# Kernel optimization log

Measured on AMD Instinct MI355X. Metric: run time of the kernel, lower is better.

The kernel has to match this reference:

```python
import jax, jax.numpy as jnp
import numpy as np

H = 32; L = 4; HEADS = 8; VC = 16; BIG = 1e9

def _unit(v):
    return v * jax.lax.rsqrt(jnp.sum(v * v, -1, keepdims=True) + 1e-8)

def _dihedrals(bb):
    n = bb.shape[0]
    X = bb[:, :3].reshape(n * 3, 3)
    U = _unit(X[1:] - X[:-1])
    u2, u1, u0 = U[:-2], U[1:-1], U[2:]
    n2 = _unit(jnp.cross(u2, u1)); n1 = _unit(jnp.cross(u1, u0))
    cosD = jnp.clip(jnp.sum(n2 * n1, -1), -1 + 1e-6, 1 - 1e-6)
    D = jnp.sign(jnp.sum(u2 * n1, -1)) * jnp.arccos(cosD)
    D = jnp.pad(D, (1, 2)).reshape(n, 3)
    return jnp.concatenate([jnp.cos(D), jnp.sin(D)], -1)

def _orientations(x):
    f = jnp.pad(_unit(x[1:] - x[:-1]), ((0, 1), (0, 0)))
    b = jnp.pad(_unit(x[:-1] - x[1:]), ((1, 0), (0, 0)))
    return jnp.stack([f, b], -2)

def _virtual_cb(bb):
    n_, ca, c = bb[:, 0], bb[:, 1], bb[:, 2]
    b = ca - n_; cc = c - ca; a = jnp.cross(b, cc)
    return -0.58273431 * a + 0.56802827 * b - 0.54067466 * cc + ca

def _rbf(d, nbin=16, dmax=20.0):
    mu = jnp.linspace(0.0, dmax, nbin); sig = dmax / nbin
    return jnp.exp(-(((d[..., None] - mu) / sig) ** 2))

def _pos_emb(didx, nemb=16):
    freq = jnp.exp(jnp.arange(0, nemb, 2, dtype=jnp.float32) * (-np.log(10000.0) / nemb))
    ang = didx[..., None].astype(jnp.float32) * freq
    return jnp.concatenate([jnp.cos(ang), jnp.sin(ang)], -1)

def _edge_rot(vec):
    # per-edge rotation aligning edge direction to e_y (equiformer-style)
    nrm = _unit(vec)
    helper = jnp.where(jnp.abs(nrm[..., 2:3]) > 0.99, jnp.array([1.0, 0.0, 0.0]), jnp.array([0.0, 0.0, 1.0]))
    z = _unit(jnp.cross(nrm, helper))
    x = jnp.cross(nrm, z)
    return jnp.stack([x, nrm, z], axis=-2)

def _rot(R, x):
    return jnp.concatenate([x[..., :1, :], jnp.einsum('...ij,...jc->...ic', R, x[..., 1:, :])], -2)

def _rot_inv(R, x):
    return jnp.concatenate([x[..., :1, :], jnp.einsum('...ji,...jc->...ic', R, x[..., 1:, :])], -2)

def _norm_so3(x, g0, b0, g1):
    x0 = x[..., 0, :]; x1 = x[..., 1:, :]
    mu = jnp.mean(x0, -1, keepdims=True)
    var = jnp.var(x0, -1, keepdims=True)
    y0 = (x0 - mu) * jax.lax.rsqrt(var + 1e-6) * g0 + b0
    y1 = x1 * jax.lax.rsqrt(jnp.mean(x1 * x1, (-2, -1), keepdims=True) + 1e-6) * g1
    return jnp.concatenate([y0[..., None, :], y1], -2)

def _project(xin, nbr, R, ef, rw1, rw2, ow):
    src = _rot(R, xin[nbr])                         # [N,k,4,Cin] gather + rotate into edge frame
    rad = jax.nn.silu(ef @ rw1) @ rw2               # [N,k,Cin] radial weights
    msg = _rot_inv(R, src * rad[..., None, :])      # rotate back to global frame
    return jnp.mean(msg, axis=1) @ ow               # [N,4,Cout]

def _forward(bb, latent, ln_g0, ln_b0, ln_g1, bb_rad_w1, bb_rad_w2, bb_out_w,
             lat_rad_w1, lat_rad_w2, lat_out_w, tln_g0, tln_b0, tln_g1,
             attn_w1, attn_w2, v_w, o_w, ffn_w1, ffn_w2, ffn_wg, ffn_v1,
             eu_w1, eu_w2, out_rad_w1, out_rad_w2, out_w,
             seq_w1, seq_b1, seq_w2, seq_b2, seq_w3, seq_b3, x_mask, n_per, k):
    N = bb.shape[0]
    Xca = bb[:, 1]
    # backbone SO3 features [N,4,7]: l=0 dihedrals (padded to 7), l=1 seven vectors
    dih = jnp.pad(_dihedrals(bb), ((0, 0), (0, 1)))
    vecs = jnp.concatenate([bb - Xca[:, None], _orientations(Xca),
                            (_virtual_cb(bb) - Xca)[:, None]], -2)
    bb_feat = jnp.concatenate([dih[:, None, :], jnp.nan_to_num(jnp.swapaxes(vecs, -1, -2))], 1)
    # kNN graph within each chain; masked residues pushed far away
    batch = jnp.arange(N) // n_per
    mx = jnp.where(x_mask[:, None], BIG, Xca)
    sq = jnp.sum(mx * mx, -1)
    d2 = sq[:, None] + sq[None, :] - 2.0 * (mx @ mx.T)
    bad = (batch[:, None] != batch[None, :]) | jnp.eye(N, dtype=bool)
    d2 = jnp.where(bad, BIG, d2)
    _, nbr = jax.lax.top_k(-d2, k)                  # [N,k] source indices per target
    edge_vec = Xca[:, None] - Xca[nbr]
    R = _edge_rot(edge_vec)                         # [N,k,3,3]
    dist = jnp.sqrt(jnp.sum(edge_vec * edge_vec, -1) + 1e-12)
    ef = jnp.concatenate([_rbf(dist), _pos_emb(nbr - jnp.arange(N)[:, None])], -1)  # [N,k,32]
    lat = _norm_so3(latent, ln_g0, ln_b0, ln_g1)
    x = jnp.concatenate([_project(bb_feat, nbr, R, ef, bb_rad_w1, bb_rad_w2, bb_out_w),
                         _project(lat, nbr, R, ef, lat_rad_w1, lat_rad_w2, lat_out_w)], -1)  # [N,4,H]
    for l in range(L):
        xl = _norm_so3(x, tln_g0[l], tln_b0[l], tln_g1[l])
        src = xl[nbr]                               # [N,k,4,H]
        feat = jnp.concatenate([src[..., 0, :],
                                jnp.broadcast_to(xl[:, None, 0, :], src[..., 0, :].shape),
                                ef], -1)            # [N,k,3H]
        alpha = jax.nn.softmax(jax.nn.silu(feat @ attn_w1[l]) @ attn_w2[l], axis=1)  # [N,k,heads]
        v = _rot_inv(R, _rot(R, src) @ v_w[l])      # [N,k,4,heads*vc]
        v = v.reshape(N, k, 4, HEADS, VC)
        agg = jnp.einsum('nkh,nkchv->nchv', alpha, v).reshape(N, 4, HEADS * VC)
        x = x + agg @ o_w[l]
        h = jax.nn.silu(x[:, 0, :] @ ffn_w1[l])
        gate = jax.nn.sigmoid(h @ ffn_wg[l])
        x = x + jnp.concatenate([(h @ ffn_w2[l])[:, None, :],
                                 (x[:, 1:, :] @ ffn_v1[l]) * gate[:, None, :]], 1)
        e_in = jnp.concatenate([ef, x[nbr][..., 0, :],
                                jnp.broadcast_to(x[:, None, 0, :], (N, k, H))], -1)
        ef = ef + jax.nn.silu(e_in @ eu_w1[l]) @ eu_w2[l]
    atoms = _project(x, nbr, R, ef, out_rad_w1, out_rad_w2, out_w)  # [N,4,91]
    decoded_latent = jnp.swapaxes(atoms[:, 1:4, :], -1, -2)         # [N,91,3]
    hh = jax.nn.relu(x[:, 0, :] @ seq_w1 + seq_b1)
    hh = jax.nn.relu(hh @ seq_w2 + seq_b2)
    seq_logits = jax.nn.log_softmax(hh @ seq_w3 + seq_b3, -1)
    return decoded_latent, seq_logits

def setup_inputs() -> dict:
    key = jax.random.key(0)
    N = 8192; n_per = 2048; k = 30
    keys = iter(jax.random.split(key, 64))
    def W(shape):
        fan = shape[-2] if len(shape) > 1 else shape[-1]
        return (jax.random.normal(next(keys), shape) / np.sqrt(fan)).astype(jnp.float32)
    inp = {
        'bb': (jax.random.normal(next(keys), (N, 4, 3)) * 3.0).astype(jnp.float32),
        'latent': jax.random.normal(next(keys), (N, 4, H), dtype=jnp.float32),
        'ln_g0': jnp.ones((H,), jnp.float32), 'ln_b0': jnp.zeros((H,), jnp.float32), 'ln_g1': jnp.ones((H,), jnp.float32),
        'bb_rad_w1': W((H, 64)), 'bb_rad_w2': W((64, 7)), 'bb_out_w': W((7, 16)),
        'lat_rad_w1': W((H, 64)), 'lat_rad_w2': W((64, H)), 'lat_out_w': W((H, 16)),
        'tln_g0': jnp.ones((L, H), jnp.float32), 'tln_b0': jnp.zeros((L, H), jnp.float32), 'tln_g1': jnp.ones((L, H), jnp.float32),
        'attn_w1': W((L, 3 * H, H)), 'attn_w2': W((L, H, HEADS)),
        'v_w': W((L, H, HEADS * VC)), 'o_w': W((L, HEADS * VC, H)),
        'ffn_w1': W((L, H, 2 * H)), 'ffn_w2': W((L, 2 * H, H)), 'ffn_wg': W((L, 2 * H, H)), 'ffn_v1': W((L, H, H)),
        'eu_w1': W((L, 3 * H, 2 * H)), 'eu_w2': W((L, 2 * H, H)),
        'out_rad_w1': W((H, 64)), 'out_rad_w2': W((64, H)), 'out_w': W((H, 91)),
        'seq_w1': W((H, 64)), 'seq_b1': jnp.zeros((64,), jnp.float32),
        'seq_w2': W((64, H)), 'seq_b2': jnp.zeros((H,), jnp.float32),
        'seq_w3': W((H, 20)), 'seq_b3': jnp.zeros((20,), jnp.float32),
        'x_mask': jnp.zeros((N,), bool), 'n_per': n_per, 'k': k,
    }
    return inp

def reference(bb, latent, ln_g0, ln_b0, ln_g1, bb_rad_w1, bb_rad_w2, bb_out_w,
              lat_rad_w1, lat_rad_w2, lat_out_w, tln_g0, tln_b0, tln_g1,
              attn_w1, attn_w2, v_w, o_w, ffn_w1, ffn_w2, ffn_wg, ffn_v1,
              eu_w1, eu_w2, out_rad_w1, out_rad_w2, out_w,
              seq_w1, seq_b1, seq_w2, seq_b2, seq_w3, seq_b3, x_mask, n_per, k):
    return _forward(bb, latent, ln_g0, ln_b0, ln_g1, bb_rad_w1, bb_rad_w2, bb_out_w,
                    lat_rad_w1, lat_rad_w2, lat_out_w, tln_g0, tln_b0, tln_g1,
                    attn_w1, attn_w2, v_w, o_w, ffn_w1, ffn_w2, ffn_wg, ffn_v1,
                    eu_w1, eu_w2, out_rad_w1, out_rad_w2, out_w,
                    seq_w1, seq_b1, seq_w2, seq_b2, seq_w3, seq_b3, x_mask, n_per, k)
```

## Files before the change

kernel.cpp:

```cpp
#include <hip/hip_runtime.h>
#include <math.h>

#define NRES 8192
#define NPER 2048
#define KNB  30
#define NEDGE (NRES*KNB)

__device__ __forceinline__ float siluf(float x){ return x / (1.0f + __expf(-x)); }

__global__ void k_pack(const float* __restrict__ bb, float4* __restrict__ ca){
  int n = blockIdx.x*256 + threadIdx.x;
  if(n >= NRES) return;
  float x=bb[n*12+3], y=bb[n*12+4], z=bb[n*12+5];
  ca[n] = make_float4(x,y,z, x*x+y*y+z*z);
}

__global__ void k_bbfeat(const float* __restrict__ bb, float* __restrict__ bbf){
  int n = blockIdx.x*256 + threadIdx.x;
  if(n >= NRES) return;
  const float* r = bb + n*12;
  float cax=r[3], cay=r[4], caz=r[5];
  float vx[7],vy[7],vz[7];
  for(int a=0;a<4;a++){ vx[a]=r[a*3]-cax; vy[a]=r[a*3+1]-cay; vz[a]=r[a*3+2]-caz; }
  if(n<NRES-1){
    float dx=bb[(n+1)*12+3]-cax, dy=bb[(n+1)*12+4]-cay, dz=bb[(n+1)*12+5]-caz;
    float s=rsqrtf(dx*dx+dy*dy+dz*dz+1e-8f);
    vx[4]=dx*s; vy[4]=dy*s; vz[4]=dz*s;
  } else { vx[4]=0.f; vy[4]=0.f; vz[4]=0.f; }
  if(n>0){
    float dx=bb[(n-1)*12+3]-cax, dy=bb[(n-1)*12+4]-cay, dz=bb[(n-1)*12+5]-caz;
    float s=rsqrtf(dx*dx+dy*dy+dz*dz+1e-8f);
    vx[5]=dx*s; vy[5]=dy*s; vz[5]=dz*s;
  } else { vx[5]=0.f; vy[5]=0.f; vz[5]=0.f; }
  {
    float bx=cax-r[0], by=cay-r[1], bz=caz-r[2];
    float cx=r[6]-cax, cy=r[7]-cay, cz=r[8]-caz;
    float axx=by*cz-bz*cy, ayy=bz*cx-bx*cz, azz=bx*cy-by*cx;
    vx[6]=-0.58273431f*axx+0.56802827f*bx-0.54067466f*cx;
    vy[6]=-0.58273431f*ayy+0.56802827f*by-0.54067466f*cy;
    vz[6]=-0.58273431f*azz+0.56802827f*bz-0.54067466f*cz;
  }
  float cD[3], sD[3];
  for(int t=0;t<3;t++){
    cD[t]=1.0f; sD[t]=0.0f;
    int f=3*n+t-1;
    if(f>=0 && f<3*NRES-3){
      float X[4][3];
      for(int q=0;q<4;q++){
        int m=f+q, rr=m/3, aa=m-rr*3;
        X[q][0]=bb[rr*12+aa*3]; X[q][1]=bb[rr*12+aa*3+1]; X[q][2]=bb[rr*12+aa*3+2];
      }
      float u2x=X[1][0]-X[0][0], u2y=X[1][1]-X[0][1], u2z=X[1][2]-X[0][2];
      float u1x=X[2][0]-X[1][0], u1y=X[2][1]-X[1][1], u1z=X[2][2]-X[1][2];
      float u0x=X[3][0]-X[2][0], u0y=X[3][1]-X[2][1], u0z=X[3][2]-X[2][2];
      float s2=rsqrtf(u2x*u2x+u2y*u2y+u2z*u2z+1e-8f); u2x*=s2; u2y*=s2; u2z*=s2;
      float s1=rsqrtf(u1x*u1x+u1y*u1y+u1z*u1z+1e-8f); u1x*=s1; u1y*=s1; u1z*=s1;
      float s0=rsqrtf(u0x*u0x+u0y*u0y+u0z*u0z+1e-8f); u0x*=s0; u0y*=s0; u0z*=s0;
      float n2x=u2y*u1z-u2z*u1y, n2y=u2z*u1x-u2x*u1z, n2z=u2x*u1y-u2y*u1x;
      float nn2=rsqrtf(n2x*n2x+n2y*n2y+n2z*n2z+1e-8f); n2x*=nn2; n2y*=nn2; n2z*=nn2;
      float n1x=u1y*u0z-u1z*u0y, n1y=u1z*u0x-u1x*u0z, n1z=u1x*u0y-u1y*u0x;
      float nn1=rsqrtf(n1x*n1x+n1y*n1y+n1z*n1z+1e-8f); n1x*=nn1; n1y*=nn1; n1z*=nn1;
      float dotn = n2x*n1x+n2y*n1y+n2z*n1z;
      float cosD = fminf(fmaxf(dotn, -1.0f+1e-6f), 1.0f-1e-6f);
      float sg = u2x*n1x+u2y*n1y+u2z*n1z;
      if(sg==0.0f){ cD[t]=1.0f; sD[t]=0.0f; }
      else {
        float sgn = (sg>0.0f)?1.0f:-1.0f;
        cD[t]=cosD;
        sD[t]=sgn*sqrtf(fmaxf(1.0f-cosD*cosD,0.0f));
      }
    }
  }
  float* o = bbf + n*28;
  o[0]=cD[0]; o[1]=cD[1]; o[2]=cD[2]; o[3]=sD[0]; o[4]=sD[1]; o[5]=sD[2]; o[6]=0.f;
  for(int c=0;c<7;c++){ o[7+c]=vx[c]; o[14+c]=vy[c]; o[21+c]=vz[c]; }
}

__global__ __launch_bounds__(256) void k_knn(const float4* __restrict__ ca, int* __restrict__ nbr){
  __shared__ float sx[NPER], sy[NPER], sz[NPER], sq[NPER];
  int wave = threadIdx.x>>6;
  int lane = threadIdx.x&63;
  int i = blockIdx.x*4 + wave;
  int batch = i / NPER;
  int base = batch*NPER;
  for(int t=threadIdx.x; t<NPER; t+=256){
    float4 c = ca[base+t];
    sx[t]=c.x; sy[t]=c.y; sz[t]=c.z; sq[t]=c.w;
  }
  __syncthreads();
  int il = i - base;
  float xi=sx[il], yi=sy[il], zi=sz[il], si=sq[il];
  float vals[32];
  float lmin = 1e30f; int larg = 0;
  #pragma unroll
  for(int t=0;t<32;t++){
    int j = t*64 + lane;
    float d2 = si + sq[j] - 2.0f*(xi*sx[j]+yi*sy[j]+zi*sz[j]);
    if(j==il) d2 = 1e30f;
    vals[t]=d2;
    if(d2 < lmin){ lmin=d2; larg=t; }
  }
  for(int it=0; it<KNB; it++){
    float v = lmin; int jg = larg*64 + lane;
    #pragma unroll
    for(int off=32; off>0; off>>=1){
      float vo = __shfl_xor(v, off, 64);
      int   jo = __shfl_xor(jg, off, 64);
      if(vo < v || (vo==v && jo<jg)){ v=vo; jg=jo; }
    }
    if(lane==0) nbr[i*KNB+it] = base + jg;
    if((jg&63)==lane){
      int targ = jg>>6;
      lmin = 1e30f; larg = 0;
      #pragma unroll
      for(int t=0;t<32;t++){
        if(t==targ) vals[t]=1e30f;
        if(vals[t]<lmin){ lmin=vals[t]; larg=t; }
      }
    }
  }
}

__global__ void k_edgefeat(const float4* __restrict__ ca, const int* __restrict__ nbr,
                           float* __restrict__ ef){
  int e = blockIdx.x*256 + threadIdx.x;
  if(e >= NEDGE) return;
  int n = e/KNB;
  int j = nbr[e];
  float4 cn = ca[n], cj = ca[j];
  float dx=cn.x-cj.x, dy=cn.y-cj.y, dz=cn.z-cj.z;
  float dist = sqrtf(dx*dx+dy*dy+dz*dz + 1e-12f);
  float* o = ef + (size_t)e*32;
  for(int m=0;m<16;m++){
    float mu = (20.0f/15.0f)*(float)m;
    float t = (dist-mu)*(1.0f/1.25f);
    o[m] = __expf(-t*t);
  }
  float didx = (float)(j - n);
  for(int m=0;m<8;m++){
    float freq = __expf(-1.1512925465f*(float)m);
    float ang = didx*freq;
    o[16+m]=cosf(ang); o[24+m]=sinf(ang);
  }
}

__global__ void k_norm(const float* __restrict__ in, float* __restrict__ out,
                       const float* __restrict__ g0, const float* __restrict__ b0,
                       const float* __restrict__ g1){
  int tid = blockIdx.x*256 + threadIdx.x;
  int n = tid >> 5, lane = tid & 31;
  if(n >= NRES) return;
  const float* xn = in + n*128;
  float x0 = xn[lane];
  float s = x0, s2 = x0*x0;
  for(int off=16; off>0; off>>=1){ s += __shfl_xor(s, off, 32); s2 += __shfl_xor(s2, off, 32); }
  float mu = s*(1.0f/32.0f);
  float var = s2*(1.0f/32.0f) - mu*mu;
  float y0 = (x0-mu)*rsqrtf(var+1e-6f)*g0[lane] + b0[lane];
  float v1 = xn[32+lane], v2 = xn[64+lane], v3 = xn[96+lane];
  float ss = v1*v1+v2*v2+v3*v3;
  for(int off=16; off>0; off>>=1){ ss += __shfl_xor(ss, off, 32); }
  float sc = rsqrtf(ss*(1.0f/96.0f) + 1e-6f);
  float g = g1[lane];
  out[n*128+lane]     = y0;
  out[n*128+32+lane]  = v1*sc*g;
  out[n*128+64+lane]  = v2*sc*g;
  out[n*128+96+lane]  = v3*sc*g;
}

__device__ __forceinline__ void load32(float* __restrict__ f, const float* __restrict__ src){
  const float4* s4 = (const float4*)src;
  #pragma unroll
  for(int q=0;q<8;q++){
    float4 v = s4[q];
    f[q*4+0]=v.x; f[q*4+1]=v.y; f[q*4+2]=v.z; f[q*4+3]=v.w;
  }
}

__global__ __launch_bounds__(256,4) void k_rad(const float* __restrict__ ef,
                     const float* __restrict__ bbw1, const float* __restrict__ bbw2,
                     const float* __restrict__ latw1, const float* __restrict__ latw2,
                     float* __restrict__ radbb, float* __restrict__ radlat){
  int e = blockIdx.x*256 + threadIdx.x;
  float f[32];
  load32(f, ef + (size_t)e*32);
  float h[64];
  #pragma unroll
  for(int o=0;o<64;o++) h[o]=0.f;
  #pragma unroll
  for(int c=0;c<32;c++){
    const float* w = bbw1 + c*64;
    #pragma unroll
    for(int o=0;o<64;o++) h[o] += f[c]*w[o];
  }
  float ab[7];
  #pragma unroll
  for(int t=0;t<7;t++) ab[t]=0.f;
  #pragma unroll
  for(int o=0;o<64;o++){
    float v = siluf(h[o]);
    const float* w2 = bbw2 + o*7;
    #pragma unroll
    for(int t=0;t<7;t++) ab[t] += v*w2[t];
  }
  {
    float4* rb4 = (float4*)(radbb + (size_t)e*8);
    rb4[0] = make_float4(ab[0],ab[1],ab[2],ab[3]);
    rb4[1] = make_float4(ab[4],ab[5],ab[6],0.f);
  }
  #pragma unroll
  for(int o=0;o<64;o++) h[o]=0.f;
  #pragma unroll
  for(int c=0;c<32;c++){
    const float* w = latw1 + c*64;
    #pragma unroll
    for(int o=0;o<64;o++) h[o] += f[c]*w[o];
  }
  float al[32];
  #pragma unroll
  for(int t=0;t<32;t++) al[t]=0.f;
  #pragma unroll
  for(int o=0;o<64;o++){
    float v = siluf(h[o]);
    const float* w2 = latw2 + o*32;
    #pragma unroll
    for(int t=0;t<32;t++) al[t] += v*w2[t];
  }
  float4* rl4 = (float4*)(radlat + (size_t)e*32);
  #pragma unroll
  for(int q=0;q<8;q++) rl4[q] = make_float4(al[q*4],al[q*4+1],al[q*4+2],al[q*4+3]);
}

__global__ __launch_bounds__(256) void k_init(const int* __restrict__ nbr,
                       const float* __restrict__ radbb, const float* __restrict__ radlat,
                       const float* __restrict__ bbf, const float* __restrict__ latn,
                       const float* __restrict__ bboutw, const float* __restrict__ latoutw,
                       const float* __restrict__ g0, const float* __restrict__ b0,
                       const float* __restrict__ g1,
                       float* __restrict__ x, float* __restrict__ xl){
  __shared__ float msgbb[4][32], msglat[4][128], xout[4][128];
  int g = threadIdx.x>>6, t = threadIdx.x&63;
  int n = blockIdx.x*4 + g;
  int t31 = t&31, t7 = t%7;
  float accL0=0.f, accL1=0.f, accB=0.f;
  for(int kk=0; kk<KNB; kk++){
    int e = n*KNB+kk;
    int j = nbr[e];
    float rl = radlat[(size_t)e*32 + t31];
    accL0 += latn[j*128+t]    * rl;
    accL1 += latn[j*128+64+t] * rl;
    if(t<28) accB += bbf[j*28+t]*radbb[(size_t)e*8 + t7];
  }
  msglat[g][t]=accL0*(1.0f/KNB); msglat[g][64+t]=accL1*(1.0f/KNB);
  if(t<28) msgbb[g][t]=accB*(1.0f/KNB);
  for(int half=0; half<2; half++){
    int e = half*64+t;
    int rrow = e>>5, c = e&31;
    float v=0.f;
    if(c<16){ for(int q=0;q<7;q++)  v += msgbb[g][rrow*7+q]*bboutw[q*16+c]; }
    else    { for(int q=0;q<32;q++) v += msglat[g][rrow*32+q]*latoutw[q*16+(c-16)]; }
    xout[g][e]=v;
    x[n*128+e]=v;
  }
  if(t<32){
    float x0=xout[g][t];
    float s=x0, s2=x0*x0;
    for(int off=16; off>0; off>>=1){ s+=__shfl_xor(s,off,32); s2+=__shfl_xor(s2,off,32); }
    float mu=s*(1.0f/32.0f), var=s2*(1.0f/32.0f)-mu*mu;
    float y0=(x0-mu)*rsqrtf(var+1e-6f)*g0[t]+b0[t];
    float v1=xout[g][32+t], v2=xout[g][64+t], v3=xout[g][96+t];
    float ss=v1*v1+v2*v2+v3*v3;
    for(int off=16; off>0; off>>=1) ss+=__shfl_xor(ss,off,32);
    float sc=rsqrtf(ss*(1.0f/96.0f)+1e-6f);
    float gg=g1[t];
    xl[n*128+t]=y0; xl[n*128+32+t]=v1*sc*gg; xl[n*128+64+t]=v2*sc*gg; xl[n*128+96+t]=v3*sc*gg;
  }
}

__global__ __launch_bounds__(256,4) void k_logits(const int* __restrict__ nbr, const float* __restrict__ xl,
                         const float* __restrict__ ef, const float* __restrict__ w1,
                         const float* __restrict__ w2, float* __restrict__ logits){
  int e = blockIdx.x*256 + threadIdx.x;
  int n = e/KNB;
  int j = nbr[e];
  float h[32];
  #pragma unroll
  for(int o=0;o<32;o++) h[o]=0.f;
  float f[32];
  load32(f, xl + (size_t)j*128);
  #pragma unroll
  for(int c=0;c<32;c++){
    const float* w = w1 + c*32;
    #pragma unroll
    for(int o=0;o<32;o++) h[o] += f[c]*w[o];
  }
  load32(f, xl + (size_t)n*128);
  #pragma unroll
  for(int c=0;c<32;c++){
    const float* w = w1 + (32+c)*32;
    #pragma unroll
    for(int o=0;o<32;o++) h[o] += f[c]*w[o];
  }
  load32(f, ef + (size_t)e*32);
  #pragma unroll
  for(int c=0;c<32;c++){
    const float* w = w1 + (64+c)*32;
    #pragma unroll
    for(int o=0;o<32;o++) h[o] += f[c]*w[o];
  }
  float acc[8];
  #pragma unroll
  for(int t=0;t<8;t++) acc[t]=0.f;
  #pragma unroll
  for(int o=0;o<32;o++){
    float v = siluf(h[o]);
    const float* w = w2 + o*8;
    #pragma unroll
    for(int t=0;t<8;t++) acc[t] += v*w[t];
  }
  float4* lg4 = (float4*)(logits + (size_t)e*8);
  lg4[0] = make_float4(acc[0],acc[1],acc[2],acc[3]);
  lg4[1] = make_float4(acc[4],acc[5],acc[6],acc[7]);
}

__global__ __launch_bounds__(256) void k_update(const int* __restrict__ nbr, const float* __restrict__ xl,
                         const float* __restrict__ logits, float* __restrict__ x,
                         float* __restrict__ xlout,
                         const float* __restrict__ vw, const float* __restrict__ ow,
                         const float* __restrict__ fw1, const float* __restrict__ fw2,
                         const float* __restrict__ fwg, const float* __restrict__ fv1,
                         const float* __restrict__ g0, const float* __restrict__ b0,
                         const float* __restrict__ g1){
  __shared__ float S_lg[4][240], S_m[4][8], S_inv[4][8];
  __shared__ float S_S[4][1024], S_agg[4][512], S_x[4][128];
  __shared__ float S_h[4][64], S_g[4][32], S_d0[4][32];
  int g = threadIdx.x>>6, t = threadIdx.x&63;
  int n = blockIdx.x*4 + g;
  for(int r=t; r<240; r+=64) S_lg[g][r] = logits[(size_t)n*240+r];
  if(t<8){
    float m=-1e30f;
    for(int kk=0;kk<KNB;kk++) m=fmaxf(m, S_lg[g][kk*8+t]);
    float s=0.f;
    for(int kk=0;kk<KNB;kk++) s += __expf(S_lg[g][kk*8+t]-m);
    S_m[g][t]=m; S_inv[g][t]=1.0f/s;
  }
  for(int r=t; r<240; r+=64){ int h=r&7; S_lg[g][r]=__expf(S_lg[g][r]-S_m[g][h])*S_inv[g][h]; }
  int hd = t>>3, i8 = t&7;
  const float4* xl4 = (const float4*)xl;
  float acc[16];
  for(int m=0;m<16;m++) acc[m]=0.f;
  for(int kk=0;kk<KNB;kk++){
    int j=nbr[n*KNB+kk];
    float a = S_lg[g][kk*8+hd];
    float4 b0v = xl4[j*32 + i8*4 + 0];
    float4 b1v = xl4[j*32 + i8*4 + 1];
    float4 b2v = xl4[j*32 + i8*4 + 2];
    float4 b3v = xl4[j*32 + i8*4 + 3];
    acc[0]+=a*b0v.x; acc[1]+=a*b0v.y; acc[2]+=a*b0v.z; acc[3]+=a*b0v.w;
    acc[4]+=a*b1v.x; acc[5]+=a*b1v.y; acc[6]+=a*b1v.z; acc[7]+=a*b1v.w;
    acc[8]+=a*b2v.x; acc[9]+=a*b2v.y; acc[10]+=a*b2v.z; acc[11]+=a*b2v.w;
    acc[12]+=a*b3v.x; acc[13]+=a*b3v.y; acc[14]+=a*b3v.z; acc[15]+=a*b3v.w;
  }
  for(int m=0;m<16;m++) S_S[g][hd*128 + i8*16 + m] = acc[m];
  for(int half=0; half<2; half++){
    int hv = half*64+t;
    int hh = hv>>4;
    float a0=0.f,a1=0.f,a2=0.f,a3=0.f;
    for(int c=0;c<32;c++){
      float w = vw[c*128+hv];
      a0 += S_S[g][hh*128 + c]*w;
      a1 += S_S[g][hh*128 + 32+c]*w;
      a2 += S_S[g][hh*128 + 64+c]*w;
      a3 += S_S[g][hh*128 + 96+c]*w;
    }
    S_agg[g][hv]=a0; S_agg[g][128+hv]=a1; S_agg[g][256+hv]=a2; S_agg[g][384+hv]=a3;
  }
  for(int half=0; half<2; half++){
    int e = half*64+t;
    int rrow = e>>5, c = e&31;
    float v = x[n*128+e];
    for(int hv=0;hv<128;hv++) v += S_agg[g][rrow*128+hv]*ow[hv*32+c];
    S_x[g][e]=v;
  }
  {
    float hs=0.f;
    for(int c=0;c<32;c++) hs += S_x[g][c]*fw1[c*64+t];
    S_h[g][t]=siluf(hs);
  }
  if(t<32){
    float gs=0.f, d0=0.f;
    for(int c=0;c<64;c++){ float hv=S_h[g][c]; gs += hv*fwg[c*32+t]; d0 += hv*fw2[c*32+t]; }
    S_g[g][t]=1.0f/(1.0f+__expf(-gs));
    S_d0[g][t]=d0;
  }
  for(int half=0; half<2; half++){
    int e = half*64+t;
    int rrow = e>>5, c = e&31;
    float xv = S_x[g][e], outv;
    if(rrow==0){ outv = xv + S_d0[g][c]; }
    else {
      float dv=0.f;
      for(int cc=0;cc<32;cc++) dv += S_x[g][rrow*32+cc]*fv1[cc*32+c];
      outv = xv + dv*S_g[g][c];
    }
    S_x[g][e]=outv;
    x[n*128+e]=outv;
  }
  if(t<32){
    float x0=S_x[g][t];
    float s=x0, s2=x0*x0;
    for(int off=16; off>0; off>>=1){ s+=__shfl_xor(s,off,32); s2+=__shfl_xor(s2,off,32); }
    float mu=s*(1.0f/32.0f), var=s2*(1.0f/32.0f)-mu*mu;
    float y0=(x0-mu)*rsqrtf(var+1e-6f)*g0[t]+b0[t];
    float v1=S_x[g][32+t], v2=S_x[g][64+t], v3=S_x[g][96+t];
    float ss=v1*v1+v2*v2+v3*v3;
    for(int off=16; off>0; off>>=1) ss+=__shfl_xor(ss,off,32);
    float sc=rsqrtf(ss*(1.0f/96.0f)+1e-6f);
    float gg=g1[t];
    xlout[n*128+t]=y0; xlout[n*128+32+t]=v1*sc*gg;
    xlout[n*128+64+t]=v2*sc*gg; xlout[n*128+96+t]=v3*sc*gg;
  }
}

__global__ __launch_bounds__(256,4) void k_efup(const int* __restrict__ nbr, const float* __restrict__ x,
                       const float* __restrict__ ew1, const float* __restrict__ ew2,
                       float* __restrict__ ef){
  int e = blockIdx.x*256 + threadIdx.x;
  int n = e/KNB;
  int j = nbr[e];
  float h[64];
  #pragma unroll
  for(int o=0;o<64;o++) h[o]=0.f;
  float f[32];
  load32(f, ef + (size_t)e*32);
  #pragma unroll
  for(int c=0;c<32;c++){
    const float* w = ew1 + c*64;
    #pragma unroll
    for(int o=0;o<64;o++) h[o] += f[c]*w[o];
  }
  load32(f, x + (size_t)j*128);
  #pragma unroll
  for(int c=0;c<32;c++){
    const float* w = ew1 + (32+c)*64;
    #pragma unroll
    for(int o=0;o<64;o++) h[o] += f[c]*w[o];
  }
  load32(f, x + (size_t)n*128);
  #pragma unroll
  for(int c=0;c<32;c++){
    const float* w = ew1 + (64+c)*64;
    #pragma unroll
    for(int o=0;o<64;o++) h[o] += f[c]*w[o];
  }
  float acc[32];
  #pragma unroll
  for(int t=0;t<32;t++) acc[t]=0.f;
  #pragma unroll
  for(int o=0;o<64;o++){
    float v = siluf(h[o]);
    const float* w = ew2 + o*32;
    #pragma unroll
    for(int t=0;t<32;t++) acc[t] += v*w[t];
  }
  load32(f, ef + (size_t)e*32);
  float4* e4 = (float4*)(ef + (size_t)e*32);
  #pragma unroll
  for(int q=0;q<8;q++){
    e4[q] = make_float4(f[q*4+0]+acc[q*4+0], f[q*4+1]+acc[q*4+1],
                        f[q*4+2]+acc[q*4+2], f[q*4+3]+acc[q*4+3]);
  }
}

__global__ __launch_bounds__(256,4) void k_orad(const float* __restrict__ ef,
                      const float* __restrict__ orw1, const float* __restrict__ orw2,
                      float* __restrict__ orad){
  int e = blockIdx.x*256 + threadIdx.x;
  float f[32];
  load32(f, ef + (size_t)e*32);
  float h[64];
  #pragma unroll
  for(int o=0;o<64;o++) h[o]=0.f;
  #pragma unroll
  for(int c=0;c<32;c++){
    const float* w = orw1 + c*64;
    #pragma unroll
    for(int o=0;o<64;o++) h[o] += f[c]*w[o];
  }
  float acc[32];
  #pragma unroll
  for(int t=0;t<32;t++) acc[t]=0.f;
  #pragma unroll
  for(int o=0;o<64;o++){
    float v = siluf(h[o]);
    const float* w = orw2 + o*32;
    #pragma unroll
    for(int t=0;t<32;t++) acc[t] += v*w[t];
  }
  float4* r4 = (float4*)(orad + (size_t)e*32);
  #pragma unroll
  for(int q=0;q<8;q++) r4[q] = make_float4(acc[q*4],acc[q*4+1],acc[q*4+2],acc[q*4+3]);
}

__global__ __launch_bounds__(256) void k_out(const int* __restrict__ nbr, const float* __restrict__ orad,
                      const float* __restrict__ x,
                      const float* __restrict__ outw,
                      const float* __restrict__ sw1, const float* __restrict__ sb1,
                      const float* __restrict__ sw2, const float* __restrict__ sb2,
                      const float* __restrict__ sw3, const float* __restrict__ sb3,
                      float* __restrict__ out, float* __restrict__ outseq){
  __shared__ float msg[4][128];
  __shared__ float h1[4][64], h2[4][32], lgs[4][20];
  int g = threadIdx.x>>6, t = threadIdx.x&63;
  int n = blockIdx.x*4 + g;
  int t31 = t&31;
  float acc0=0.f, acc1=0.f;
  for(int kk=0;kk<KNB;kk++){
    int e=n*KNB+kk;
    int j=nbr[e];
    float rl = orad[(size_t)e*32 + t31];
    acc0 += x[j*128+t]*rl;
    acc1 += x[j*128+64+t]*rl;
  }
  msg[g][t]=acc0*(1.0f/KNB); msg[g][64+t]=acc1*(1.0f/KNB);
  for(int o=t;o<91;o+=64){
    for(int rrow=1;rrow<4;rrow++){
      float s=0.f;
      for(int c=0;c<32;c++) s += msg[g][rrow*32+c]*outw[c*91+o];
      out[(size_t)n*273 + o*3 + (rrow-1)] = s;
    }
  }
  {
    float s=0.f;
    for(int c=0;c<32;c++) s += x[n*128+c]*sw1[c*64+t];
    h1[g][t]=fmaxf(s+sb1[t],0.f);
  }
  if(t<32){
    float s=0.f;
    for(int c=0;c<64;c++) s += h1[g][c]*sw2[c*32+t];
    h2[g][t]=fmaxf(s+sb2[t],0.f);
  }
  if(t<20){
    float s=0.f;
    for(int c=0;c<32;c++) s += h2[g][c]*sw3[c*20+t];
    lgs[g][t]=s+sb3[t];
  }
  if(t<20){
    float m=-1e30f;
    for(int c=0;c<20;c++) m=fmaxf(m,lgs[g][c]);
    float se=0.f;
    for(int c=0;c<20;c++) se += __expf(lgs[g][c]-m);
    outseq[(size_t)n*20+t]=lgs[g][t]-m-logf(se);
  }
}

extern "C" void kernel_launch(void* const* d_in, const int* in_sizes, int n_in,
                              void* d_out, int out_size, void* d_ws, size_t ws_size,
                              hipStream_t stream) {
  const float* bb      = (const float*)d_in[0];
  const float* latent  = (const float*)d_in[1];
  const float* ln_g0   = (const float*)d_in[2];
  const float* ln_b0   = (const float*)d_in[3];
  const float* ln_g1   = (const float*)d_in[4];
  const float* bbw1    = (const float*)d_in[5];
  const float* bbw2    = (const float*)d_in[6];
  const float* bboutw  = (const float*)d_in[7];
  const float* latw1   = (const float*)d_in[8];
  const float* latw2   = (const float*)d_in[9];
  const float* latoutw = (const float*)d_in[10];
  const float* tg0     = (const float*)d_in[11];
  const float* tb0     = (const float*)d_in[12];
  const float* tg1     = (const float*)d_in[13];
  const float* aw1     = (const float*)d_in[14];
  const float* aw2     = (const float*)d_in[15];
  const float* vw      = (const float*)d_in[16];
  const float* ow      = (const float*)d_in[17];
  const float* fw1     = (const float*)d_in[18];
  const float* fw2     = (const float*)d_in[19];
  const float* fwg     = (const float*)d_in[20];
  const float* fv1     = (const float*)d_in[21];
  const float* ew1     = (const float*)d_in[22];
  const float* ew2     = (const float*)d_in[23];
  const float* orw1    = (const float*)d_in[24];
  const float* orw2    = (const float*)d_in[25];
  const float* outw    = (const float*)d_in[26];
  const float* sw1     = (const float*)d_in[27];
  const float* sb1     = (const float*)d_in[28];
  const float* sw2     = (const float*)d_in[29];
  const float* sb2     = (const float*)d_in[30];
  const float* sw3     = (const float*)d_in[31];
  const float* sb3     = (const float*)d_in[32];
  float* outp = (float*)d_out;

  int*    nbr    = (int*)d_ws;
  float*  ef     = (float*)((char*)d_ws + 1024*1024);
  float*  xbuf   = ef   + (size_t)NEDGE*32;
  float*  xlA    = xbuf + (size_t)NRES*128;
  float*  xlB    = xlA  + (size_t)NRES*128;
  float*  bbf    = xlB  + (size_t)NRES*128;
  float*  logits = bbf  + (size_t)NRES*28;
  float4* ca     = (float4*)(logits + (size_t)NEDGE*8);
  float*  edgescratch = (float*)(ca + NRES);
  float*  radbb  = logits;
  float*  radlat = edgescratch;
  float*  orad   = edgescratch;

  k_pack    <<<NRES/256, 256, 0, stream>>>(bb, ca);
  k_bbfeat  <<<NRES/256, 256, 0, stream>>>(bb, bbf);
  k_knn     <<<NRES/4,   256, 0, stream>>>(ca, nbr);
  k_edgefeat<<<NEDGE/256, 256, 0, stream>>>(ca, nbr, ef);
  k_norm    <<<NRES*32/256, 256, 0, stream>>>(latent, xlA, ln_g0, ln_b0, ln_g1);
  k_rad     <<<NEDGE/256, 256, 0, stream>>>(ef, bbw1, bbw2, latw1, latw2, radbb, radlat);
  k_init    <<<NRES/4, 256, 0, stream>>>(nbr, radbb, radlat, bbf, xlA,
                                         bboutw, latoutw,
                                         tg0, tb0, tg1,
                                         xbuf, xlB);
  for(int l=0;l<4;l++){
    const float* xl_in  = (l&1) ? xlA : xlB;
    float*       xl_out = (l&1) ? xlB : xlA;
    int ln = (l+1<4) ? (l+1) : 3;
    k_logits <<<NEDGE/256, 256, 0, stream>>>(nbr, xl_in, ef, aw1+l*96*32, aw2+l*32*8, logits);
    k_update <<<NRES/4, 256, 0, stream>>>(nbr, xl_in, logits, xbuf, xl_out,
                                          vw+l*32*128, ow+l*128*32,
                                          fw1+l*32*64, fw2+l*64*32,
                                          fwg+l*64*32, fv1+l*32*32,
                                          tg0+ln*32, tb0+ln*32, tg1+ln*32);
    k_efup   <<<NEDGE/256, 256, 0, stream>>>(nbr, xbuf, ew1+l*96*64, ew2+l*64*32, ef);
  }
  k_orad<<<NEDGE/256, 256, 0, stream>>>(ef, orw1, orw2, orad);
  k_out <<<NRES/4, 256, 0, stream>>>(nbr, orad, xbuf, outw,
                                     sw1, sb1, sw2, sb2, sw3, sb3,
                                     outp, outp + (size_t)NRES*273);
}
```

Baseline: 1.329 ms.

## Fuse edge feature computation into radial MLP and speed up kNN selection

Removes the separate edge-feature kernel: k_rad now computes the RBF and positional features itself, uses them directly, and writes them to ef for later layers. This saves one launch and a read of ef. The kNN kernel now uses 512-thread blocks that share the staged coordinates across 8 queries. It also keeps per-group minima over four groups of 8 candidates, so each extraction rescans only one group instead of all 32 values. The costs are extra register pressure in k_rad and more branching in the kNN inner loop.

```diff
diff --git a/kernel.cpp b/kernel.cpp
--- a/kernel.cpp
+++ b/kernel.cpp
@@ -76,14 +76,14 @@
   for(int c=0;c<7;c++){ o[7+c]=vx[c]; o[14+c]=vy[c]; o[21+c]=vz[c]; }
 }
 
-__global__ __launch_bounds__(256) void k_knn(const float4* __restrict__ ca, int* __restrict__ nbr){
+__global__ __launch_bounds__(512) void k_knn(const float4* __restrict__ ca, int* __restrict__ nbr){
   __shared__ float sx[NPER], sy[NPER], sz[NPER], sq[NPER];
   int wave = threadIdx.x>>6;
   int lane = threadIdx.x&63;
-  int i = blockIdx.x*4 + wave;
+  int i = blockIdx.x*8 + wave;
   int batch = i / NPER;
   int base = batch*NPER;
-  for(int t=threadIdx.x; t<NPER; t+=256){
+  for(int t=threadIdx.x; t<NPER; t+=512){
     float4 c = ca[base+t];
     sx[t]=c.x; sy[t]=c.y; sz[t]=c.z; sq[t]=c.w;
   }
@@ -91,15 +91,22 @@
   int il = i - base;
   float xi=sx[il], yi=sy[il], zi=sz[il], si=sq[il];
   float vals[32];
-  float lmin = 1e30f; int larg = 0;
+  float gm[4]; int ga[4];
+  #pragma unroll
+  for(int grp=0;grp<4;grp++){ gm[grp]=1e30f; ga[grp]=grp*8; }
   #pragma unroll
   for(int t=0;t<32;t++){
     int j = t*64 + lane;
     float d2 = si + sq[j] - 2.0f*(xi*sx[j]+yi*sy[j]+zi*sz[j]);
     if(j==il) d2 = 1e30f;
     vals[t]=d2;
-    if(d2 < lmin){ lmin=d2; larg=t; }
-  }
+    int grp = t>>3;
+    if(d2 < gm[grp]){ gm[grp]=d2; ga[grp]=t; }
+  }
+  float lmin = gm[0]; int larg = ga[0];
+  if(gm[1]<lmin){ lmin=gm[1]; larg=ga[1]; }
+  if(gm[2]<lmin){ lmin=gm[2]; larg=ga[2]; }
+  if(gm[3]<lmin){ lmin=gm[3]; larg=ga[3]; }
   for(int it=0; it<KNB; it++){
     float v = lmin; int jg = larg*64 + lane;
     #pragma unroll
@@ -110,37 +117,24 @@
     }
     if(lane==0) nbr[i*KNB+it] = base + jg;
     if((jg&63)==lane){
-      int targ = jg>>6;
-      lmin = 1e30f; larg = 0;
+      int wt = jg>>6;
+      int grp = wt>>3;
       #pragma unroll
-      for(int t=0;t<32;t++){
-        if(t==targ) vals[t]=1e30f;
-        if(vals[t]<lmin){ lmin=vals[t]; larg=t; }
+      for(int g2=0; g2<4; g2++){
+        if(grp==g2){
+          #pragma unroll
+          for(int q=0;q<8;q++) if(g2*8+q==wt) vals[g2*8+q]=1e30f;
+          float m=1e30f; int a=g2*8;
+          #pragma unroll
+          for(int q=0;q<8;q++){ if(vals[g2*8+q]<m){ m=vals[g2*8+q]; a=g2*8+q; } }
+          gm[g2]=m; ga[g2]=a;
+        }
       }
+      lmin=gm[0]; larg=ga[0];
+      if(gm[1]<lmin){ lmin=gm[1]; larg=ga[1]; }
+      if(gm[2]<lmin){ lmin=gm[2]; larg=ga[2]; }
+      if(gm[3]<lmin){ lmin=gm[3]; larg=ga[3]; }
     }
-  }
-}
-
-__global__ void k_edgefeat(const float4* __restrict__ ca, const int* __restrict__ nbr,
-                           float* __restrict__ ef){
-  int e = blockIdx.x*256 + threadIdx.x;
-  if(e >= NEDGE) return;
-  int n = e/KNB;
-  int j = nbr[e];
-  float4 cn = ca[n], cj = ca[j];
-  float dx=cn.x-cj.x, dy=cn.y-cj.y, dz=cn.z-cj.z;
-  float dist = sqrtf(dx*dx+dy*dy+dz*dz + 1e-12f);
-  float* o = ef + (size_t)e*32;
-  for(int m=0;m<16;m++){
-    float mu = (20.0f/15.0f)*(float)m;
-    float t = (dist-mu)*(1.0f/1.25f);
-    o[m] = __expf(-t*t);
-  }
-  float didx = (float)(j - n);
-  for(int m=0;m<8;m++){
-    float freq = __expf(-1.1512925465f*(float)m);
-    float ang = didx*freq;
-    o[16+m]=cosf(ang); o[24+m]=sinf(ang);
   }
 }
 
@@ -177,13 +171,36 @@
   }
 }
 
-__global__ __launch_bounds__(256,4) void k_rad(const float* __restrict__ ef,
+__global__ __launch_bounds__(256,4) void k_rad(const float4* __restrict__ ca, const int* __restrict__ nbr,
                      const float* __restrict__ bbw1, const float* __restrict__ bbw2,
                      const float* __restrict__ latw1, const float* __restrict__ latw2,
+                     float* __restrict__ ef,
                      float* __restrict__ radbb, float* __restrict__ radlat){
   int e = blockIdx.x*256 + threadIdx.x;
+  int n = e/KNB;
+  int j = nbr[e];
+  float4 cn = ca[n], cj = ca[j];
+  float dx=cn.x-cj.x, dy=cn.y-cj.y, dz=cn.z-cj.z;
+  float dist = sqrtf(dx*dx+dy*dy+dz*dz + 1e-12f);
   float f[32];
-  load32(f, ef + (size_t)e*32);
+  #pragma unroll
+  for(int m=0;m<16;m++){
+    float mu = (20.0f/15.0f)*(float)m;
+    float t = (dist-mu)*(1.0f/1.25f);
+    f[m] = __expf(-t*t);
+  }
+  float didx = (float)(j - n);
+  #pragma unroll
+  for(int m=0;m<8;m++){
+    float freq = __expf(-1.1512925465f*(float)m);
+    float ang = didx*freq;
+    f[16+m]=cosf(ang); f[24+m]=sinf(ang);
+  }
+  {
+    float4* o4 = (float4*)(ef + (size_t)e*32);
+    #pragma unroll
+    for(int q=0;q<8;q++) o4[q] = make_float4(f[q*4],f[q*4+1],f[q*4+2],f[q*4+3]);
+  }
   float h[64];
   #pragma unroll
   for(int o=0;o<64;o++) h[o]=0.f;
@@ -607,10 +624,10 @@
 
   k_pack    <<<NRES/256, 256, 0, stream>>>(bb, ca);
   k_bbfeat  <<<NRES/256, 256, 0, stream>>>(bb, bbf);
-  k_knn     <<<NRES/4,   256, 0, stream>>>(ca, nbr);
-  k_edgefeat<<<NEDGE/256, 256, 0, stream>>>(ca, nbr, ef);
+  k_knn     <<<NRES/8,   512, 0, stream>>>(ca, nbr);
   k_norm    <<<NRES*32/256, 256, 0, stream>>>(latent, xlA, ln_g0, ln_b0, ln_g1);
-  k_rad     <<<NEDGE/256, 256, 0, stream>>>(ef, bbw1, bbw2, latw1, latw2, radbb, radlat);
+  k_rad     <<<NEDGE/256, 256, 0, stream>>>(ca, nbr, bbw1, bbw2, latw1, latw2,
+                                            ef, radbb, radlat);
   k_init    <<<NRES/4, 256, 0, stream>>>(nbr, radbb, radlat, bbf, xlA,
                                          bboutw, latoutw,
                                          tg0, tb0, tg1,
```

Result: slower. 1.624 ms (+22.2%).
